# Performance work log

Hardware: AMD Instinct MI355X
Metric: run time of the kernel (lower is better)

Reference implementation:

```python
import jax, jax.numpy as jnp
import numpy as np

EMBED = 1024
HEADS = 16
HEAD_DIM = EMBED // HEADS
FFN_DIM = 4096
SEQ = 2048
BATCH = 2
EPS = 1e-5


def setup_inputs() -> dict:
    key = jax.random.key(0)
    ks = jax.random.split(key, 13)
    s = lambda n: 1.0 / np.sqrt(n)
    return {
        "x": jax.random.normal(ks[0], (BATCH, SEQ, EMBED), jnp.float32),
        # qkv projection (stored as [in, out])
        "w_qkv": jax.random.normal(ks[1], (EMBED, 3 * EMBED), jnp.float32) * s(EMBED),
        "b_qkv": jax.random.normal(ks[2], (3 * EMBED,), jnp.float32) * 0.02,
        "w_out": jax.random.normal(ks[3], (EMBED, EMBED), jnp.float32) * s(EMBED),
        "b_out": jax.random.normal(ks[4], (EMBED,), jnp.float32) * 0.02,
        # FFN
        "w_up": jax.random.normal(ks[5], (EMBED, FFN_DIM), jnp.float32) * s(EMBED),
        "b_up": jax.random.normal(ks[6], (FFN_DIM,), jnp.float32) * 0.02,
        "w_down": jax.random.normal(ks[7], (FFN_DIM, EMBED), jnp.float32) * s(FFN_DIM),
        "b_down": jax.random.normal(ks[8], (EMBED,), jnp.float32) * 0.02,
        # LayerNorms
        "g1": jnp.ones((EMBED,), jnp.float32),
        "be1": jnp.zeros((EMBED,), jnp.float32),
        "g2": jnp.ones((EMBED,), jnp.float32),
        "be2": jnp.zeros((EMBED,), jnp.float32),
    }


def _layernorm(x, g, b):
    mu = jnp.mean(x, axis=-1, keepdims=True)
    var = jnp.mean(jnp.square(x - mu), axis=-1, keepdims=True)
    return (x - mu) * jax.lax.rsqrt(var + EPS) * g + b


def reference(x, w_qkv, b_qkv, w_out, b_out, w_up, b_up, w_down, b_down, g1, be1, g2, be2):
    B, S, E = x.shape
    qkv = (x @ w_qkv + b_qkv).reshape(B, S, 3, HEADS, HEAD_DIM)
    qkv = jnp.transpose(qkv, (2, 0, 3, 1, 4))
    q, k, v = qkv[0], qkv[1], qkv[2]
    scale = 1.0 / jnp.sqrt(jnp.float32(HEAD_DIM))
    attn = jnp.einsum("bhqd,bhkd->bhqk", q, k) * scale  # [B,H,S,S]
    causal = jnp.tril(jnp.ones((S, S), bool))
    attn = jnp.where(causal, attn, -jnp.inf)
    attn = jax.nn.softmax(attn, axis=-1)
    out = jnp.einsum("bhqk,bhkd->bhqd", attn, v)  # [B,H,S,D]
    out = jnp.transpose(out, (0, 2, 1, 3)).reshape(B, S, E)
    attn_out = out @ w_out + b_out
    x = _layernorm(x + attn_out, g1, be1)
    ffn_out = jax.nn.relu(x @ w_up + b_up) @ w_down + b_down
    return _layernorm(x + ffn_out, g2, be2)
```

## Files before the change

### kernel.cpp

```cpp
#include <hip/hip_runtime.h>
#include <hip/hip_bf16.h>

#define EMBED 1024
#define HEADS 16
#define HDIM 64
#define FFN 4096
#define SEQ 2048
#define BATCH 2
#define MTOT (BATCH*SEQ)
#define QSCALE 0.1803368801111137f

typedef __attribute__((ext_vector_type(8))) short bf16x8;
typedef __attribute__((ext_vector_type(4))) float f32x4;
typedef __attribute__((ext_vector_type(16))) float f32x16;
typedef unsigned short u16;
typedef unsigned int u32;

__device__ __forceinline__ u16 f2bf(float f) {
  union { float f; unsigned u; } v; v.f = f;
  unsigned r = v.u + 0x7FFFu + ((v.u >> 16) & 1u);
  return (u16)(r >> 16);
}

__device__ __forceinline__ void async_ld16(const void* g, void* l) {
  __builtin_amdgcn_global_load_lds((const __attribute__((address_space(1))) void*)g,
                                   (__attribute__((address_space(3))) void*)l,
                                   16, 0, 0);
}

__global__ __launch_bounds__(256) void k_cvt(const float* __restrict__ in,
                                             u16* __restrict__ out, int n4) {
  int i = blockIdx.x * 256 + threadIdx.x;
  int st = gridDim.x * 256;
  for (; i < n4; i += st) {
    float4 v = ((const float4*)in)[i];
    ushort4 o;
    o.x = f2bf(v.x); o.y = f2bf(v.y); o.z = f2bf(v.z); o.w = f2bf(v.w);
    ((ushort4*)out)[i] = o;
  }
}

__global__ __launch_bounds__(256) void k_tr(const float* __restrict__ w,
                                            u16* __restrict__ wT, int K, int N) {
  __shared__ u16 tile[32][33];
  int n0 = blockIdx.x * 32, k0 = blockIdx.y * 32;
  int tx = threadIdx.x, ty = threadIdx.y;
  #pragma unroll
  for (int i = 0; i < 4; ++i) {
    int k = k0 + ty + i * 8;
    tile[ty + i * 8][tx] = f2bf(w[(size_t)k * N + n0 + tx]);
  }
  __syncthreads();
  #pragma unroll
  for (int i = 0; i < 4; ++i) {
    int n = n0 + ty + i * 8;
    wT[(size_t)n * K + k0 + tx] = tile[tx][ty + i * 8];
  }
}

__global__ __launch_bounds__(256) void k_vtr(const u16* __restrict__ V,
                                             u16* __restrict__ Vt) {
  __shared__ u16 t[64][72];
  const int s0 = blockIdx.x * 64;
  const size_t ib = (size_t)blockIdx.y * (size_t)SEQ * HDIM;
  const size_t ob = (size_t)blockIdx.y * (size_t)HDIM * SEQ;
  const int tid = threadIdx.x;
  const int r = tid >> 2, c0 = (tid & 3) * 16;
  bf16x8 v0 = *(const bf16x8*)(V + ib + (size_t)(s0 + r) * HDIM + c0);
  bf16x8 v1 = *(const bf16x8*)(V + ib + (size_t)(s0 + r) * HDIM + c0 + 8);
  #pragma unroll
  for (int j = 0; j < 8; ++j) {
    t[c0 + j][r] = (u16)v0[j];
    t[c0 + 8 + j][r] = (u16)v1[j];
  }
  __syncthreads();
  const int d = tid >> 2, sc = (tid & 3) * 16;
  bf16x8 o0, o1;
  #pragma unroll
  for (int j = 0; j < 8; ++j) { o0[j] = t[d][sc + j]; o1[j] = t[d][sc + 8 + j]; }
  *(bf16x8*)(Vt + ob + (size_t)d * SEQ + s0 + sc) = o0;
  *(bf16x8*)(Vt + ob + (size_t)d * SEQ + s0 + sc + 8) = o1;
}

template <int BN, int BK, int OMODE, bool RELU>
__global__ __launch_bounds__(256) void k_gemm(
    const u16* __restrict__ A, const u16* __restrict__ BT,
    const float* __restrict__ bias,
    void* __restrict__ out0, void* __restrict__ out1, void* __restrict__ out2,
    int M, int N, int K) {
  constexpr int NR = BN / 32;
  constexpr int KS = BK / 32;
  constexpr int TPR = BK / 8;
  constexpr int RPI = 256 / TPR;
  constexpr int CM = TPR - 1;

  __shared__ u16 As[2][128 * BK];
  __shared__ u16 Bs[2][BN * BK];
  const int tid = threadIdx.x;
  const int lane = tid & 63, g = lane >> 4, li = lane & 15;
  const int wid = tid >> 6, wm = wid >> 1, wn = wid & 1;
  const int m0 = blockIdx.y * 128, n0 = blockIdx.x * BN;

  f32x4 acc[4][NR] = {};

  const u16* Ablk = A + (size_t)m0 * K;
  const u16* Bblk = BT + (size_t)n0 * K;
  const int srow = tid / TPR;
  const int scol = ((tid % TPR) ^ (srow & CM)) * 8;

  auto stage = [&](int buf, int kt) {
    #pragma unroll
    for (int r = 0; r < 128; r += RPI)
      async_ld16(Ablk + (size_t)(srow + r) * K + kt + scol, &As[buf][(srow + r) * BK] + (tid % TPR) * 8);
    #pragma unroll
    for (int r = 0; r < BN; r += RPI)
      async_ld16(Bblk + (size_t)(srow + r) * K + kt + scol, &Bs[buf][(srow + r) * BK] + (tid % TPR) * 8);
  };

  stage(0, 0);
  int cur = 0;
  for (int kt = 0; kt < K; kt += BK) {
    __syncthreads();
    if (kt + BK < K) stage(cur ^ 1, kt + BK);

    bf16x8 af[4][KS], bfr[NR][KS];
    #pragma unroll
    for (int i = 0; i < 4; ++i) {
      const int row = wm * 64 + i * 16 + li;
      #pragma unroll
      for (int ks = 0; ks < KS; ++ks) {
        const int c = ks * 4 + g;
        af[i][ks] = *(const bf16x8*)(&As[cur][row * BK] + ((c ^ (row & CM)) & CM) * 8);
      }
    }
    #pragma unroll
    for (int j = 0; j < NR; ++j) {
      const int row = wn * (BN / 2) + j * 16 + li;
      #pragma unroll
      for (int ks = 0; ks < KS; ++ks) {
        const int c = ks * 4 + g;
        bfr[j][ks] = *(const bf16x8*)(&Bs[cur][row * BK] + ((c ^ (row & CM)) & CM) * 8);
      }
    }
    #pragma unroll
    for (int ks = 0; ks < KS; ++ks)
      #pragma unroll
      for (int i = 0; i < 4; ++i)
        #pragma unroll
        for (int j = 0; j < NR; ++j)
          acc[i][j] = __builtin_amdgcn_mfma_f32_16x16x32_bf16(af[i][ks], bfr[j][ks], acc[i][j], 0, 0, 0);
    cur ^= 1;
  }

  float bcol[NR];
  #pragma unroll
  for (int j = 0; j < NR; ++j) bcol[j] = bias[n0 + wn * (BN / 2) + j * 16 + li];

  #pragma unroll
  for (int i = 0; i < 4; ++i) {
    #pragma unroll
    for (int j = 0; j < NR; ++j) {
      #pragma unroll
      for (int r = 0; r < 4; ++r) {
        int row = m0 + wm * 64 + i * 16 + g * 4 + r;
        int col = n0 + wn * (BN / 2) + j * 16 + li;
        float v = acc[i][j][r] + bcol[j];
        if (RELU) v = fmaxf(v, 0.f);
        if (OMODE == 0) {
          ((u16*)out0)[(size_t)row * N + col] = f2bf(v);
        } else if (OMODE == 1) {
          ((float*)out0)[(size_t)row * N + col] = v;
        } else {
          int which = col >> 10, hh = (col >> 6) & 15, d = col & 63;
          int bb = row >> 11, ss = row & 2047;
          if (which == 0) v *= QSCALE;
          u16* dst = which == 0 ? (u16*)out0 : (which == 1 ? (u16*)out1 : (u16*)out2);
          dst[((size_t)((bb * 16 + hh) * 2048 + ss)) * 64 + d] = f2bf(v);
        }
      }
    }
  }
}

__global__ __launch_bounds__(256) void k_attn3(
    const u16* __restrict__ Q, const u16* __restrict__ K,
    const u16* __restrict__ Vt, u16* __restrict__ ctx) {
  const int bh = blockIdx.x;
  const int z  = blockIdx.y;
  const int qb = (z < 8) ? (2 * z) : (31 - 2 * z);
  const int b = bh >> 4, h = bh & 15;
  const int tid = threadIdx.x;
  const int wid = tid >> 6, lane = tid & 63;
  const int ql = lane & 31, hl = lane >> 5;

  __shared__ u16 Ks[2][64 * 64];
  __shared__ u16 Vs[2][64 * 64];

  const size_t kbase = (size_t)bh * SEQ * HDIM;
  const size_t vbase = (size_t)bh * HDIM * SEQ;
  const int wq0 = qb * 128 + wid * 32;
  const int qg = wq0 + ql;

  bf16x8 qf[4];
  #pragma unroll
  for (int d4 = 0; d4 < 4; ++d4)
    qf[d4] = *(const bf16x8*)(Q + kbase + (size_t)qg * HDIM + d4 * 16 + hl * 8);

  f32x16 o0 = {}, o1 = {};
  float m_run = -1e30f, l_run = 0.f;

  const int srow = tid >> 3;
  const int scol = ((tid & 7) ^ (srow & 7)) * 8;

  auto stage = [&](int buf, int t2) {
    const u16* kg = K + kbase + (size_t)(t2 * 64 + srow) * HDIM + scol;
    async_ld16(kg, &Ks[buf][0] + tid * 8);
    async_ld16(kg + (size_t)32 * HDIM, &Ks[buf][0] + 2048 + tid * 8);
    const u16* vg = Vt + vbase + (size_t)srow * SEQ + t2 * 64 + scol;
    async_ld16(vg, &Vs[buf][0] + tid * 8);
    async_ld16(vg + (size_t)32 * SEQ, &Vs[buf][0] + 2048 + tid * 8);
  };

  const int ntiles = 2 * qb + 2;
  stage(0, 0);
  int cur = 0;

  for (int kt = 0; kt < ntiles; ++kt) {
    __syncthreads();
    if (kt + 1 < ntiles) stage(cur ^ 1, kt + 1);

    if (kt * 64 <= wq0 + 31) {
      const bool kh1 = (kt * 64 + 32 <= wq0 + 31);
      const bool domask = (kt * 64 + (kh1 ? 63 : 31) > wq0);

      f32x16 S0 = {}, S1 = {};
      #pragma unroll
      for (int d4 = 0; d4 < 4; ++d4) {
        bf16x8 kf = *(const bf16x8*)(&Ks[cur][0] + ql * 64 + (((2 * d4 + hl) ^ (ql & 7)) * 8));
        S0 = __builtin_amdgcn_mfma_f32_32x32x16_bf16(kf, qf[d4], S0, 0, 0, 0);
      }
      if (kh1) {
        #pragma unroll
        for (int d4 = 0; d4 < 4; ++d4) {
          const int row = 32 + ql;
          bf16x8 kf = *(const bf16x8*)(&Ks[cur][0] + row * 64 + (((2 * d4 + hl) ^ (row & 7)) * 8));
          S1 = __builtin_amdgcn_mfma_f32_32x32x16_bf16(kf, qf[d4], S1, 0, 0, 0);
        }
      }

      if (domask) {
        const int qrel = qg - kt * 64 - 4 * hl;
        #pragma unroll
        for (int r = 0; r < 16; ++r) {
          const int kc = (r & 3) + 8 * (r >> 2);
          S0[r] = (kc <= qrel) ? S0[r] : -3.0e38f;
        }
        if (kh1) {
          #pragma unroll
          for (int r = 0; r < 16; ++r) {
            const int kc = 32 + (r & 3) + 8 * (r >> 2);
            S1[r] = (kc <= qrel) ? S1[r] : -3.0e38f;
          }
        }
      }

      float mt = -3.0e38f;
      #pragma unroll
      for (int r = 0; r < 16; ++r) mt = fmaxf(mt, S0[r]);
      if (kh1) {
        #pragma unroll
        for (int r = 0; r < 16; ++r) mt = fmaxf(mt, S1[r]);
      }
      mt = fmaxf(mt, __shfl_xor(mt, 32, 64));
      const float mn = fmaxf(m_run, mt);
      const float alpha = exp2f(m_run - mn);
      float sum = 0.f;
      #pragma unroll
      for (int r = 0; r < 16; ++r) { S0[r] = exp2f(S0[r] - mn); sum += S0[r]; }
      if (kh1) {
        #pragma unroll
        for (int r = 0; r < 16; ++r) { S1[r] = exp2f(S1[r] - mn); sum += S1[r]; }
      }
      sum += __shfl_xor(sum, 32, 64);
      l_run = l_run * alpha + sum;
      m_run = mn;
      o0 *= alpha;
      o1 *= alpha;

      u32 pk[2][8], sw[2][8];
      #pragma unroll
      for (int m = 0; m < 4; ++m) {
        asm("v_cvt_pk_bf16_f32 %0, %1, %2" : "=v"(pk[0][2*m])   : "v"(S0[4*m+0]), "v"(S0[4*m+1]));
        asm("v_cvt_pk_bf16_f32 %0, %1, %2" : "=v"(pk[0][2*m+1]) : "v"(S0[4*m+2]), "v"(S0[4*m+3]));
      }
      #pragma unroll
      for (int i = 0; i < 8; ++i) sw[0][i] = __shfl_xor(pk[0][i], 32, 64);
      if (kh1) {
        #pragma unroll
        for (int m = 0; m < 4; ++m) {
          asm("v_cvt_pk_bf16_f32 %0, %1, %2" : "=v"(pk[1][2*m])   : "v"(S1[4*m+0]), "v"(S1[4*m+1]));
          asm("v_cvt_pk_bf16_f32 %0, %1, %2" : "=v"(pk[1][2*m+1]) : "v"(S1[4*m+2]), "v"(S1[4*m+3]));
        }
        #pragma unroll
        for (int i = 0; i < 8; ++i) sw[1][i] = __shfl_xor(pk[1][i], 32, 64);
      }

      #pragma unroll
      for (int t = 0; t < 4; ++t) {
        if (t < 2 || kh1) {
          const int c = t >> 1, m0 = 2 * (t & 1), m1 = m0 + 1;
          union { u32 u[4]; bf16x8 v; } pf;
          pf.u[0] = hl ? sw[c][2*m1]   : pk[c][2*m0];
          pf.u[1] = hl ? sw[c][2*m1+1] : pk[c][2*m0+1];
          pf.u[2] = hl ? pk[c][2*m1]   : sw[c][2*m0];
          pf.u[3] = hl ? pk[c][2*m1+1] : sw[c][2*m0+1];
          {
            bf16x8 vf = *(const bf16x8*)(&Vs[cur][0] + ql * 64 + (((2 * t + hl) ^ (ql & 7)) * 8));
            o0 = __builtin_amdgcn_mfma_f32_32x32x16_bf16(vf, pf.v, o0, 0, 0, 0);
          }
          {
            const int row = 32 + ql;
            bf16x8 vf = *(const bf16x8*)(&Vs[cur][0] + row * 64 + (((2 * t + hl) ^ (row & 7)) * 8));
            o1 = __builtin_amdgcn_mfma_f32_32x32x16_bf16(vf, pf.v, o1, 0, 0, 0);
          }
        }
      }
    }
    cur ^= 1;
  }

  const float inv = 1.f / l_run;
  u16* outp = ctx + (size_t)(b * SEQ + qg) * EMBED + h * HDIM + 4 * hl;
  #pragma unroll
  for (int m = 0; m < 4; ++m) {
    ushort4 s0v, s1v;
    s0v.x = f2bf(o0[4*m+0] * inv); s0v.y = f2bf(o0[4*m+1] * inv);
    s0v.z = f2bf(o0[4*m+2] * inv); s0v.w = f2bf(o0[4*m+3] * inv);
    *(ushort4*)(outp + 8 * m) = s0v;
    s1v.x = f2bf(o1[4*m+0] * inv); s1v.y = f2bf(o1[4*m+1] * inv);
    s1v.z = f2bf(o1[4*m+2] * inv); s1v.w = f2bf(o1[4*m+3] * inv);
    *(ushort4*)(outp + 32 + 8 * m) = s1v;
  }
}

__global__ __launch_bounds__(256) void k_add_ln(
    const float* __restrict__ a, const float* __restrict__ bmat,
    const float* __restrict__ gam, const float* __restrict__ bet,
    float* __restrict__ outf, u16* __restrict__ outb) {
  const int row = blockIdx.x;
  const int t = threadIdx.x;
  __shared__ float red[8];
  float4 va = ((const float4*)(a + (size_t)row * EMBED))[t];
  float4 vb = ((const float4*)(bmat + (size_t)row * EMBED))[t];
  float s0 = va.x + vb.x, s1 = va.y + vb.y, s2 = va.z + vb.z, s3 = va.w + vb.w;
  float sum = s0 + s1 + s2 + s3;
  float sq = s0 * s0 + s1 * s1 + s2 * s2 + s3 * s3;
  #pragma unroll
  for (int m = 1; m < 64; m <<= 1) {
    sum += __shfl_xor(sum, m, 64);
    sq += __shfl_xor(sq, m, 64);
  }
  int wid = t >> 6;
  if ((t & 63) == 0) { red[wid] = sum; red[4 + wid] = sq; }
  __syncthreads();
  sum = red[0] + red[1] + red[2] + red[3];
  sq = red[4] + red[5] + red[6] + red[7];
  float mean = sum * (1.f / EMBED);
  float var = sq * (1.f / EMBED) - mean * mean;
  float rstd = rsqrtf(var + 1e-5f);
  float4 gv = ((const float4*)gam)[t], bev = ((const float4*)bet)[t];
  float y0 = (s0 - mean) * rstd * gv.x + bev.x;
  float y1 = (s1 - mean) * rstd * gv.y + bev.y;
  float y2 = (s2 - mean) * rstd * gv.z + bev.z;
  float y3 = (s3 - mean) * rstd * gv.w + bev.w;
  float4 o; o.x = y0; o.y = y1; o.z = y2; o.w = y3;
  ((float4*)(outf + (size_t)row * EMBED))[t] = o;
  if (outb) {
    ushort4 ob; ob.x = f2bf(y0); ob.y = f2bf(y1); ob.z = f2bf(y2); ob.w = f2bf(y3);
    ((ushort4*)(outb + (size_t)row * EMBED))[t] = ob;
  }
}

extern "C" void kernel_launch(void* const* d_in, const int* in_sizes, int n_in,
                              void* d_out, int out_size, void* d_ws, size_t ws_size,
                              hipStream_t stream) {
  const float* x      = (const float*)d_in[0];
  const float* w_qkv  = (const float*)d_in[1];
  const float* b_qkv  = (const float*)d_in[2];
  const float* w_out  = (const float*)d_in[3];
  const float* b_out  = (const float*)d_in[4];
  const float* w_up   = (const float*)d_in[5];
  const float* b_up   = (const float*)d_in[6];
  const float* w_down = (const float*)d_in[7];
  const float* b_down = (const float*)d_in[8];
  const float* g1  = (const float*)d_in[9];
  const float* be1 = (const float*)d_in[10];
  const float* g2  = (const float*)d_in[11];
  const float* be2 = (const float*)d_in[12];

  char* ws = (char*)d_ws;
  size_t off = 0;
  auto alloc = [&](size_t bytes) { void* p = ws + off; off += (bytes + 255) & ~(size_t)255; return p; };

  u16* xb     = (u16*)alloc((size_t)MTOT * EMBED * 2);
  u16* wqkvT  = (u16*)alloc((size_t)3 * EMBED * EMBED * 2);
  u16* woutT  = (u16*)alloc((size_t)EMBED * EMBED * 2);
  u16* wupT   = (u16*)alloc((size_t)FFN * EMBED * 2);
  u16* wdownT = (u16*)alloc((size_t)EMBED * FFN * 2);
  u16* qb     = (u16*)alloc((size_t)MTOT * EMBED * 2);
  u16* kb     = (u16*)alloc((size_t)MTOT * EMBED * 2);
  u16* vb     = (u16*)alloc((size_t)MTOT * EMBED * 2);
  u16* vtb    = (u16*)alloc((size_t)MTOT * EMBED * 2);
  u16* ctx    = (u16*)alloc((size_t)MTOT * EMBED * 2);
  float* attn_proj = (float*)alloc((size_t)MTOT * EMBED * 4);
  float* y_f32     = (float*)alloc((size_t)MTOT * EMBED * 4);
  u16* y_bf16      = (u16*)alloc((size_t)MTOT * EMBED * 2);
  u16* hmid        = (u16*)alloc((size_t)MTOT * FFN * 2);
  float* ffn_o     = (float*)alloc((size_t)MTOT * EMBED * 4);

  dim3 trb(32, 8);
  k_cvt<<<2048, 256, 0, stream>>>(x, xb, MTOT * EMBED / 4);
  k_tr<<<dim3(3 * EMBED / 32, EMBED / 32), trb, 0, stream>>>(w_qkv, wqkvT, EMBED, 3 * EMBED);
  k_tr<<<dim3(EMBED / 32, EMBED / 32), trb, 0, stream>>>(w_out, woutT, EMBED, EMBED);
  k_tr<<<dim3(FFN / 32, EMBED / 32), trb, 0, stream>>>(w_up, wupT, EMBED, FFN);
  k_tr<<<dim3(EMBED / 32, FFN / 32), trb, 0, stream>>>(w_down, wdownT, FFN, EMBED);

  k_gemm<128, 32, 2, false><<<dim3(3 * EMBED / 128, MTOT / 128), 256, 0, stream>>>(
      xb, wqkvT, b_qkv, qb, kb, vb, MTOT, 3 * EMBED, EMBED);

  k_vtr<<<dim3(SEQ / 64, BATCH * HEADS), 256, 0, stream>>>(vb, vtb);

  k_attn3<<<dim3(BATCH * HEADS, 16), 256, 0, stream>>>(qb, kb, vtb, ctx);

  k_gemm<64, 64, 1, false><<<dim3(EMBED / 64, MTOT / 128), 256, 0, stream>>>(
      ctx, woutT, b_out, attn_proj, nullptr, nullptr, MTOT, EMBED, EMBED);

  k_add_ln<<<MTOT, 256, 0, stream>>>(x, attn_proj, g1, be1, y_f32, y_bf16);

  k_gemm<128, 32, 0, true><<<dim3(FFN / 128, MTOT / 128), 256, 0, stream>>>(
      y_bf16, wupT, b_up, hmid, nullptr, nullptr, MTOT, FFN, EMBED);

  k_gemm<64, 64, 1, false><<<dim3(EMBED / 64, MTOT / 128), 256, 0, stream>>>(
      hmid, wdownT, b_down, ffn_o, nullptr, nullptr, MTOT, EMBED, FFN);

  k_add_ln<<<MTOT, 256, 0, stream>>>(y_f32, ffn_o, g2, be2, (float*)d_out, nullptr);

  (void)in_sizes; (void)n_in; (void)out_size; (void)ws_size;
}
```

Measured before the change: 279.9 us.

## Drop LDS staging in attention; load K/V per-wave from global with interleaved query tiles

Measured after the change: 280.3 us. About the same (+0.2%).

```diff
diff --git a/kernel.cpp b/kernel.cpp
--- a/kernel.cpp
+++ b/kernel.cpp
@@ -182,151 +182,135 @@
   }
 }
 
-__global__ __launch_bounds__(256) void k_attn3(
+__global__ __launch_bounds__(256, 3) void k_attn4(
     const u16* __restrict__ Q, const u16* __restrict__ K,
     const u16* __restrict__ Vt, u16* __restrict__ ctx) {
   const int bh = blockIdx.x;
   const int z  = blockIdx.y;
-  const int qb = (z < 8) ? (2 * z) : (31 - 2 * z);
   const int b = bh >> 4, h = bh & 15;
   const int tid = threadIdx.x;
   const int wid = tid >> 6, lane = tid & 63;
   const int ql = lane & 31, hl = lane >> 5;
 
-  __shared__ u16 Ks[2][64 * 64];
-  __shared__ u16 Vs[2][64 * 64];
+  const int s = z * 4 + wid;
+  const int t32 = (s & 1) ? (63 - (s >> 1)) : (s >> 1);
+  const int wq0 = t32 * 32;
+  const int qg = wq0 + ql;
 
   const size_t kbase = (size_t)bh * SEQ * HDIM;
   const size_t vbase = (size_t)bh * HDIM * SEQ;
-  const int wq0 = qb * 128 + wid * 32;
-  const int qg = wq0 + ql;
 
   bf16x8 qf[4];
   #pragma unroll
   for (int d4 = 0; d4 < 4; ++d4)
     qf[d4] = *(const bf16x8*)(Q + kbase + (size_t)qg * HDIM + d4 * 16 + hl * 8);
 
+  const u16* kp = K + kbase + (size_t)ql * HDIM + hl * 8;
+  const u16* vp = Vt + vbase + (size_t)ql * SEQ + hl * 8;
+
   f32x16 o0 = {}, o1 = {};
   float m_run = -1e30f, l_run = 0.f;
 
-  const int srow = tid >> 3;
-  const int scol = ((tid & 7) ^ (srow & 7)) * 8;
-
-  auto stage = [&](int buf, int t2) {
-    const u16* kg = K + kbase + (size_t)(t2 * 64 + srow) * HDIM + scol;
-    async_ld16(kg, &Ks[buf][0] + tid * 8);
-    async_ld16(kg + (size_t)32 * HDIM, &Ks[buf][0] + 2048 + tid * 8);
-    const u16* vg = Vt + vbase + (size_t)srow * SEQ + t2 * 64 + scol;
-    async_ld16(vg, &Vs[buf][0] + tid * 8);
-    async_ld16(vg + (size_t)32 * SEQ, &Vs[buf][0] + 2048 + tid * 8);
-  };
-
-  const int ntiles = 2 * qb + 2;
-  stage(0, 0);
-  int cur = 0;
-
+  const int ntiles = (wq0 + 31) / 64 + 1;
   for (int kt = 0; kt < ntiles; ++kt) {
-    __syncthreads();
-    if (kt + 1 < ntiles) stage(cur ^ 1, kt + 1);
-
-    if (kt * 64 <= wq0 + 31) {
-      const bool kh1 = (kt * 64 + 32 <= wq0 + 31);
-      const bool domask = (kt * 64 + (kh1 ? 63 : 31) > wq0);
-
-      f32x16 S0 = {}, S1 = {};
-      #pragma unroll
-      for (int d4 = 0; d4 < 4; ++d4) {
-        bf16x8 kf = *(const bf16x8*)(&Ks[cur][0] + ql * 64 + (((2 * d4 + hl) ^ (ql & 7)) * 8));
-        S0 = __builtin_amdgcn_mfma_f32_32x32x16_bf16(kf, qf[d4], S0, 0, 0, 0);
+    const bool kh1 = (kt * 64 + 32 <= wq0 + 31);
+    const bool domask = (kt * 64 + (kh1 ? 63 : 31) > wq0);
+    const int koff = kt * 64 * HDIM;
+
+    bf16x8 kf0[4], kf1[4];
+    #pragma unroll
+    for (int d4 = 0; d4 < 4; ++d4) {
+      kf0[d4] = *(const bf16x8*)(kp + koff + d4 * 16);
+      if (kh1) kf1[d4] = *(const bf16x8*)(kp + koff + 32 * HDIM + d4 * 16);
+    }
+    bf16x8 vf0[4], vf1[4];
+    #pragma unroll
+    for (int t = 0; t < 4; ++t)
+      if (t < 2 || kh1) {
+        vf0[t] = *(const bf16x8*)(vp + kt * 64 + t * 16);
+        vf1[t] = *(const bf16x8*)(vp + 32 * SEQ + kt * 64 + t * 16);
+      }
+
+    f32x16 S0 = {}, S1 = {};
+    #pragma unroll
+    for (int d4 = 0; d4 < 4; ++d4)
+      S0 = __builtin_amdgcn_mfma_f32_32x32x16_bf16(kf0[d4], qf[d4], S0, 0, 0, 0);
+    if (kh1) {
+      #pragma unroll
+      for (int d4 = 0; d4 < 4; ++d4)
+        S1 = __builtin_amdgcn_mfma_f32_32x32x16_bf16(kf1[d4], qf[d4], S1, 0, 0, 0);
+    }
+
+    if (domask) {
+      const int qrel = qg - kt * 64 - 4 * hl;
+      #pragma unroll
+      for (int r = 0; r < 16; ++r) {
+        const int kc = (r & 3) + 8 * (r >> 2);
+        S0[r] = (kc <= qrel) ? S0[r] : -3.0e38f;
       }
       if (kh1) {
         #pragma unroll
-        for (int d4 = 0; d4 < 4; ++d4) {
-          const int row = 32 + ql;
-          bf16x8 kf = *(const bf16x8*)(&Ks[cur][0] + row * 64 + (((2 * d4 + hl) ^ (row & 7)) * 8));
-          S1 = __builtin_amdgcn_mfma_f32_32x32x16_bf16(kf, qf[d4], S1, 0, 0, 0);
+        for (int r = 0; r < 16; ++r) {
+          const int kc = 32 + (r & 3) + 8 * (r >> 2);
+          S1[r] = (kc <= qrel) ? S1[r] : -3.0e38f;
         }
       }
-
-      if (domask) {
-        const int qrel = qg - kt * 64 - 4 * hl;
-        #pragma unroll
-        for (int r = 0; r < 16; ++r) {
-          const int kc = (r & 3) + 8 * (r >> 2);
-          S0[r] = (kc <= qrel) ? S0[r] : -3.0e38f;
-        }
-        if (kh1) {
-          #pragma unroll
-          for (int r = 0; r < 16; ++r) {
-            const int kc = 32 + (r & 3) + 8 * (r >> 2);
-            S1[r] = (kc <= qrel) ? S1[r] : -3.0e38f;
-          }
-        }
-      }
-
-      float mt = -3.0e38f;
-      #pragma unroll
-      for (int r = 0; r < 16; ++r) mt = fmaxf(mt, S0[r]);
-      if (kh1) {
-        #pragma unroll
-        for (int r = 0; r < 16; ++r) mt = fmaxf(mt, S1[r]);
-      }
-      mt = fmaxf(mt, __shfl_xor(mt, 32, 64));
-      const float mn = fmaxf(m_run, mt);
-      const float alpha = exp2f(m_run - mn);
-      float sum = 0.f;
-      #pragma unroll
-      for (int r = 0; r < 16; ++r) { S0[r] = exp2f(S0[r] - mn); sum += S0[r]; }
-      if (kh1) {
-        #pragma unroll
-        for (int r = 0; r < 16; ++r) { S1[r] = exp2f(S1[r] - mn); sum += S1[r]; }
-      }
-      sum += __shfl_xor(sum, 32, 64);
-      l_run = l_run * alpha + sum;
-      m_run = mn;
-      o0 *= alpha;
-      o1 *= alpha;
-
-      u32 pk[2][8], sw[2][8];
+    }
+
+    float mt = -3.0e38f;
+    #pragma unroll
+    for (int r = 0; r < 16; ++r) mt = fmaxf(mt, S0[r]);
+    if (kh1) {
+      #pragma unroll
+      for (int r = 0; r < 16; ++r) mt = fmaxf(mt, S1[r]);
+    }
+    mt = fmaxf(mt, __shfl_xor(mt, 32, 64));
+    const float mn = fmaxf(m_run, mt);
+    const float alpha = exp2f(m_run - mn);
+    float sum = 0.f;
+    #pragma unroll
+    for (int r = 0; r < 16; ++r) { S0[r] = exp2f(S0[r] - mn); sum += S0[r]; }
+    if (kh1) {
+      #pragma unroll
+      for (int r = 0; r < 16; ++r) { S1[r] = exp2f(S1[r] - mn); sum += S1[r]; }
+    }
+    sum += __shfl_xor(sum, 32, 64);
+    l_run = l_run * alpha + sum;
+    m_run = mn;
+    o0 *= alpha;
+    o1 *= alpha;
+
+    u32 pk[2][8], sw[2][8];
+    #pragma unroll
+    for (int m = 0; m < 4; ++m) {
+      asm("v_cvt_pk_bf16_f32 %0, %1, %2" : "=v"(pk[0][2*m])   : "v"(S0[4*m+0]), "v"(S0[4*m+1]));
+      asm("v_cvt_pk_bf16_f32 %0, %1, %2" : "=v"(pk[0][2*m+1]) : "v"(S0[4*m+2]), "v"(S0[4*m+3]));
+    }
+    #pragma unroll
+    for (int i = 0; i < 8; ++i) sw[0][i] = __shfl_xor(pk[0][i], 32, 64);
+    if (kh1) {
       #pragma unroll
       for (int m = 0; m < 4; ++m) {
-        asm("v_cvt_pk_bf16_f32 %0, %1, %2" : "=v"(pk[0][2*m])   : "v"(S0[4*m+0]), "v"(S0[4*m+1]));
-        asm("v_cvt_pk_bf16_f32 %0, %1, %2" : "=v"(pk[0][2*m+1]) : "v"(S0[4*m+2]), "v"(S0[4*m+3]));
-      }
-      #pragma unroll
-      for (int i = 0; i < 8; ++i) sw[0][i] = __shfl_xor(pk[0][i], 32, 64);
-      if (kh1) {
-        #pragma unroll
-        for (int m = 0; m < 4; ++m) {
-          asm("v_cvt_pk_bf16_f32 %0, %1, %2" : "=v"(pk[1][2*m])   : "v"(S1[4*m+0]), "v"(S1[4*m+1]));
-          asm("v_cvt_pk_bf16_f32 %0, %1, %2" : "=v"(pk[1][2*m+1]) : "v"(S1[4*m+2]), "v"(S1[4*m+3]));
-        }
-        #pragma unroll
-        for (int i = 0; i < 8; ++i) sw[1][i] = __shfl_xor(pk[1][i], 32, 64);
-      }
-
-      #pragma unroll
-      for (int t = 0; t < 4; ++t) {
-        if (t < 2 || kh1) {
-          const int c = t >> 1, m0 = 2 * (t & 1), m1 = m0 + 1;
-          union { u32 u[4]; bf16x8 v; } pf;
-          pf.u[0] = hl ? sw[c][2*m1]   : pk[c][2*m0];
-          pf.u[1] = hl ? sw[c][2*m1+1] : pk[c][2*m0+1];
-          pf.u[2] = hl ? pk[c][2*m1]   : sw[c][2*m0];
-          pf.u[3] = hl ? pk[c][2*m1+1] : sw[c][2*m0+1];
-          {
-            bf16x8 vf = *(const bf16x8*)(&Vs[cur][0] + ql * 64 + (((2 * t + hl) ^ (ql & 7)) * 8));
-            o0 = __builtin_amdgcn_mfma_f32_32x32x16_bf16(vf, pf.v, o0, 0, 0, 0);
-          }
-          {
-            const int row = 32 + ql;
-            bf16x8 vf = *(const bf16x8*)(&Vs[cur][0] + row * 64 + (((2 * t + hl) ^ (row & 7)) * 8));
-            o1 = __builtin_amdgcn_mfma_f32_32x32x16_bf16(vf, pf.v, o1, 0, 0, 0);
-          }
-        }
-      }
-    }
-    cur ^= 1;
+        asm("v_cvt_pk_bf16_f32 %0, %1, %2" : "=v"(pk[1][2*m])   : "v"(S1[4*m+0]), "v"(S1[4*m+1]));
+        asm("v_cvt_pk_bf16_f32 %0, %1, %2" : "=v"(pk[1][2*m+1]) : "v"(S1[4*m+2]), "v"(S1[4*m+3]));
+      }
+      #pragma unroll
+      for (int i = 0; i < 8; ++i) sw[1][i] = __shfl_xor(pk[1][i], 32, 64);
+    }
+
+    #pragma unroll
+    for (int t = 0; t < 4; ++t) {
+      if (t < 2 || kh1) {
+        const int c = t >> 1, m0 = 2 * (t & 1), m1 = m0 + 1;
+        union { u32 u[4]; bf16x8 v; } pf;
+        pf.u[0] = hl ? sw[c][2*m1]   : pk[c][2*m0];
+        pf.u[1] = hl ? sw[c][2*m1+1] : pk[c][2*m0+1];
+        pf.u[2] = hl ? pk[c][2*m1]   : sw[c][2*m0];
+        pf.u[3] = hl ? pk[c][2*m1+1] : sw[c][2*m0+1];
+        o0 = __builtin_amdgcn_mfma_f32_32x32x16_bf16(vf0[t], pf.v, o0, 0, 0, 0);
+        o1 = __builtin_amdgcn_mfma_f32_32x32x16_bf16(vf1[t], pf.v, o1, 0, 0, 0);
+      }
+    }
   }
 
   const float inv = 1.f / l_run;
@@ -430,7 +414,7 @@
 
   k_vtr<<<dim3(SEQ / 64, BATCH * HEADS), 256, 0, stream>>>(vb, vtb);
 
-  k_attn3<<<dim3(BATCH * HEADS, 16), 256, 0, stream>>>(qb, kb, vtb, ctx);
+  k_attn4<<<dim3(BATCH * HEADS, 16), 256, 0, stream>>>(qb, kb, vtb, ctx);
 
   k_gemm<64, 64, 1, false><<<dim3(EMBED / 64, MTOT / 128), 256, 0, stream>>>(
       ctx, woutT, b_out, attn_proj, nullptr, nullptr, MTOT, EMBED, EMBED);
```
